# Optimization experiments

Measured on AMD Instinct MI355X. Metric: run time of the kernel, lower is better.

## Reference

```python
import jax, jax.numpy as jnp
import numpy as np

N, K, DN, DA, H = 20000, 16, 128, 128, 256
D_IN = DN + DA  # 256


def _lin_init(key, out_dim, in_dim):
    scale = 1.0 / np.sqrt(in_dim)
    return jax.random.uniform(key, (out_dim, in_dim), jnp.float32, -scale, scale)


def setup_inputs() -> dict:
    key = jax.random.key(0)
    ks = jax.random.split(key, 16)
    # adjacency: col 0 = parent index; cols 1..K = neighbor indices, -1 padded.
    parent = jax.random.randint(ks[0], (N, 1), 0, N, dtype=jnp.int32)
    nbr_first = jax.random.randint(ks[1], (N, 1), 0, N, dtype=jnp.int32)  # guarantee >=1 nbr
    nbr_rest = jax.random.randint(ks[2], (N, K - 1), -1, N, dtype=jnp.int32)
    adj = jnp.concatenate([parent, nbr_first, nbr_rest], axis=1)
    names = jax.random.normal(ks[3], (N, DN), jnp.float32)
    attrs = jax.random.normal(ks[4], (N, DA), jnp.float32)
    return {
        "nodeAdjacencySpecTensor": adj,
        "nodeNamesEncoded": names,
        "nodeAttributesEncoded": attrs,
        "W_in": _lin_init(ks[5], H, D_IN),
        "b_in": jnp.zeros((H,), jnp.float32),
        "W_parent": _lin_init(ks[6], H, H),
        "b_parent": jnp.zeros((H,), jnp.float32),
        "W_neighbor": _lin_init(ks[7], H, H),
        "b_neighbor": jnp.zeros((H,), jnp.float32),
        "W_ih": _lin_init(ks[8], 3 * H, H),
        "b_ih": jnp.zeros((3 * H,), jnp.float32),
        "W_hh": _lin_init(ks[9], 3 * H, H),
        "b_hh": jnp.zeros((3 * H,), jnp.float32),
        "depth": 3,
    }


def _gru_cell(x, h, W_ih, b_ih, W_hh, b_hh):
    # torch.nn.GRUCell math; gate order r, z, n.
    gi = x @ W_ih.T + b_ih
    gh = h @ W_hh.T + b_hh
    i_r, i_z, i_n = jnp.split(gi, 3, axis=-1)
    h_r, h_z, h_n = jnp.split(gh, 3, axis=-1)
    r = jax.nn.sigmoid(i_r + h_r)
    z = jax.nn.sigmoid(i_z + h_z)
    n = jnp.tanh(i_n + r * h_n)
    return (1.0 - z) * n + z * h


def reference(nodeAdjacencySpecTensor, nodeNamesEncoded, nodeAttributesEncoded,
              W_in, b_in, W_parent, b_parent, W_neighbor, b_neighbor,
              W_ih, b_ih, W_hh, b_hh, depth):
    adj = nodeAdjacencySpecTensor
    parent_idx = adj[:, 0]                 # [N]
    nbr_idx = adj[:, 1:]                   # [N, K], -1 padded
    mask = (nbr_idx >= 0)                  # [N, K]
    safe_nbr = jnp.clip(nbr_idx, 0, None)
    nbr_count = jnp.maximum(mask.sum(axis=1), 1).astype(jnp.float32)  # [N]

    node_info = jnp.concatenate([nodeNamesEncoded, nodeAttributesEncoded], axis=-1)
    x = node_info @ W_in.T + b_in          # [N, H]

    for _ in range(depth):
        p = x @ W_parent.T + b_parent      # [N, H]
        nbr = x @ W_neighbor.T + b_neighbor  # [N, H]
        # irregular gathers
        parent_feat = p[parent_idx]        # [N, H]
        gathered = nbr[safe_nbr]           # [N, K, H]
        nbr_sum = jnp.sum(gathered * mask[:, :, None], axis=1)  # [N, H]
        summary = parent_feat + nbr_sum / nbr_count[:, None]
        x = _gru_cell(x, summary, W_ih, b_ih, W_hh, b_hh)
    return x
```

## Files before the change

kernel.cpp:

```cpp
#include <hip/hip_runtime.h>
#include <hip/hip_bf16.h>

typedef __bf16 bf16x8 __attribute__((ext_vector_type(8)));
typedef __bf16 bf16x4 __attribute__((ext_vector_type(4)));
typedef float  f32x4  __attribute__((ext_vector_type(4)));

#define NN   20000
#define NADJ 17

__device__ __forceinline__ void xcd_remap(int b, int nwg, int col_shift, int& r, int& c)
{
    int q = nwg >> 3, rem = nwg & 7;
    int x = b & 7, k = b >> 3;
    int start = x * q + (x < rem ? x : rem);
    int idx = start + k;
    r = idx >> col_shift;
    c = idx & ((1 << col_shift) - 1);
}

__global__ void pack_weights_kernel(const float* __restrict__ Win, const float* __restrict__ bin,
                                    const float* __restrict__ Wp,  const float* __restrict__ bp,
                                    const float* __restrict__ Wn,  const float* __restrict__ bn,
                                    const float* __restrict__ Wih, const float* __restrict__ bih,
                                    const float* __restrict__ Whh, const float* __restrict__ bhh,
                                    __bf16* __restrict__ Wb, float* __restrict__ bc)
{
    int idx = blockIdx.x * 256 + threadIdx.x;
    if (idx < 1536) {
        int c = idx; float v;
        if (c < 256)      v = bin[c];
        else if (c < 512) { int j = c - 256; v = bp[j] + bn[j]; }
        else {
            int rel = c - 512;
            int j = (rel >> 6) * 16 + (rel & 15);
            int g = (rel >> 4) & 3;
            if      (g == 0) v = bih[j] + bhh[j];
            else if (g == 1) v = bih[256 + j] + bhh[256 + j];
            else if (g == 2) v = bih[512 + j];
            else             v = bhh[512 + j];
        }
        bc[c] = v;
    }
    if (idx >= 180224) return;
    int e = idx << 2;
    const float* src = nullptr;
    bool zero = false;
    if (e < 65536) {
        int row = e >> 8, k = e & 255;
        src = Win + (size_t)row * 256 + k;
    } else if (e < 196608) {
        int rel = e - 65536;
        int row = rel >> 9, k = rel & 511;
        src = (k < 256) ? (Wp + (size_t)row * 256 + k)
                        : (Wn + (size_t)row * 256 + (k - 256));
    } else {
        int rel = e - 196608;
        int row = rel >> 9, k = rel & 511;
        int j = (row >> 6) * 16 + (row & 15);
        int g = (row >> 4) & 3;
        if (k < 256) {
            if (g == 3) zero = true;
            else {
                int off = (g == 0) ? 0 : (g == 1) ? 256 : 512;
                src = Wih + (size_t)(off + j) * 256 + k;
            }
        } else {
            int k2 = k - 256;
            if (g == 2) zero = true;
            else {
                int off = (g == 0) ? 0 : (g == 1) ? 256 : 512;
                src = Whh + (size_t)(off + j) * 256 + k2;
            }
        }
    }
    float4 v = zero ? make_float4(0.f, 0.f, 0.f, 0.f) : *(const float4*)src;
    bf16x4 o = { (__bf16)v.x, (__bf16)v.y, (__bf16)v.z, (__bf16)v.w };
    *(bf16x4*)(Wb + (size_t)e) = o;
}

__global__ void pack_info_kernel(const float* __restrict__ names, const float* __restrict__ attrs,
                                 __bf16* __restrict__ xb)
{
    int idx = blockIdx.x * 256 + threadIdx.x;
    if (idx >= NN * 64) return;
    int i  = idx >> 6;
    int d4 = (idx & 63) << 2;
    const float* src = (d4 < 128) ? (names + (size_t)i * 128 + d4)
                                  : (attrs + (size_t)i * 128 + (d4 - 128));
    float4 v = *(const float4*)src;
    bf16x4 o = { (__bf16)v.x, (__bf16)v.y, (__bf16)v.z, (__bf16)v.w };
    *(bf16x4*)(xb + (size_t)i * 256 + d4) = o;
}

__global__ void gather_avg_kernel(const int* __restrict__ adj, const __bf16* __restrict__ x,
                                  __bf16* __restrict__ G2)
{
    const int l  = threadIdx.x & 63;
    const int w  = threadIdx.x >> 6;
    const int lh = l & 31;
    const int node = blockIdx.x * 8 + w * 2 + (l >> 5);
    int av = (lh < NADJ) ? adj[(size_t)node * NADJ + lh] : -1;
    float s[8] = {0.f, 0.f, 0.f, 0.f, 0.f, 0.f, 0.f, 0.f};
    int cnt = 0;
#pragma unroll
    for (int j = 1; j < NADJ; ++j) {
        int idx = __shfl(av, (l & 32) + j, 64);
        if (idx >= 0) {
            ++cnt;
            bf16x8 v = *(const bf16x8*)(x + (size_t)idx * 256 + lh * 8);
#pragma unroll
            for (int u = 0; u < 8; ++u) s[u] += (float)v[u];
        }
    }
    float inv = 1.f / (float)(cnt < 1 ? 1 : cnt);
    bf16x8 o;
#pragma unroll
    for (int u = 0; u < 8; ++u) o[u] = (__bf16)(s[u] * inv);
    *(bf16x8*)(G2 + (size_t)node * 256 + lh * 8) = o;
}

#define PIPE_BARRIER()                                \
    do {                                              \
        asm volatile("" ::: "memory");                \
        __builtin_amdgcn_s_barrier();                 \
        asm volatile("" ::: "memory");                \
    } while (0)

__global__ __launch_bounds__(512, 4)
void gemm_bias_kernel(const __bf16* __restrict__ A0, const __bf16* __restrict__ A1, int lda,
                      const int* __restrict__ parents, int par_stride,
                      const __bf16* __restrict__ W, int ldw,
                      const float* __restrict__ bias,
                      __bf16* __restrict__ Cb, __bf16* __restrict__ Cl,
                      int n_rows, int n_cols, int kt_n, int nwg, int col_shift)
{
    __shared__ __align__(16) __bf16 As[2][128 * 64];
    __shared__ __align__(16) __bf16 Bs[2][128 * 64];
    __shared__ int par_s[128];
    const int t = threadIdx.x;
    const int w = t >> 6;
    const int l = t & 63;
    int rb, cb_;
    xcd_remap(blockIdx.x, nwg, col_shift, rb, cb_);
    const int brow = rb * 128;
    const int bcol = cb_ * 128;
    const int wr = (w >> 1) * 32, wc = (w & 1) * 64;

    if (parents) {
        if (t < 128) {
            int node = brow + t; if (node > n_rows - 1) node = n_rows - 1;
            par_s[t] = parents[(size_t)node * par_stride];
        }
        __syncthreads();
    }

    auto stage = [&](int kt, int buf) {
        const int k0 = kt * 64;
#pragma unroll
        for (int i = 0; i < 2; ++i) {
            int f   = i * 512 + t;
            int row = f >> 3;
            int cs  = ((f & 7) * 16) ^ ((row & 7) << 4);
            int ar  = brow + row; if (ar > n_rows - 1) ar = n_rows - 1;
            const __bf16* abase;
            if (parents && k0 < 256)             abase = A0 + (size_t)par_s[row] * 256 + k0;
            else if (A1 != nullptr && k0 >= 256) abase = A1 + (size_t)ar * 256 + (k0 - 256);
            else                                 abase = A0 + (size_t)ar * lda + k0;
            const __bf16* ga = abase + (cs >> 1);
            char* la = (char*)As[buf] + (i * 512 + w * 64) * 16;
            __builtin_amdgcn_global_load_lds(
                (const __attribute__((address_space(1))) unsigned int*)ga,
                (__attribute__((address_space(3))) unsigned int*)la, 16, 0, 0);
        }
#pragma unroll
        for (int i = 0; i < 2; ++i) {
            int f   = i * 512 + t;
            int row = f >> 3;
            int cs  = ((f & 7) * 16) ^ ((row & 7) << 4);
            const __bf16* gb = W + (size_t)(bcol + row) * ldw + k0 + (cs >> 1);
            char* lb = (char*)Bs[buf] + (i * 512 + w * 64) * 16;
            __builtin_amdgcn_global_load_lds(
                (const __attribute__((address_space(1))) unsigned int*)gb,
                (__attribute__((address_space(3))) unsigned int*)lb, 16, 0, 0);
        }
    };

    f32x4 acc[2][4] = {};
    stage(0, 0);

    for (int kt = 0; kt < kt_n; ++kt) {
        const int buf = kt & 1;
        if (kt + 1 < kt_n) {
            stage(kt + 1, buf ^ 1);
            asm volatile("s_waitcnt vmcnt(4)" ::: "memory");
        } else {
            asm volatile("s_waitcnt vmcnt(0)" ::: "memory");
        }
        PIPE_BARRIER();
#pragma unroll
        for (int ks = 0; ks < 2; ++ks) {
            bf16x8 af[2], bfv[4];
#pragma unroll
            for (int m = 0; m < 2; ++m) {
                int row = wr + m * 16 + (l & 15);
                int cb  = (ks * 64 + ((l >> 4) * 16)) ^ ((row & 7) << 4);
                af[m] = *(const bf16x8*)((const char*)As[buf] + row * 128 + cb);
            }
#pragma unroll
            for (int n = 0; n < 4; ++n) {
                int row = wc + n * 16 + (l & 15);
                int cb  = (ks * 64 + ((l >> 4) * 16)) ^ ((row & 7) << 4);
                bfv[n] = *(const bf16x8*)((const char*)Bs[buf] + row * 128 + cb);
            }
#pragma unroll
            for (int m = 0; m < 2; ++m)
#pragma unroll
                for (int n = 0; n < 4; ++n)
                    acc[m][n] = __builtin_amdgcn_mfma_f32_16x16x32_bf16(af[m], bfv[n], acc[m][n], 0, 0, 0);
        }
        PIPE_BARRIER();
    }
#pragma unroll
    for (int m = 0; m < 2; ++m) {
        int r0 = brow + wr + m * 16 + ((l >> 4) * 4);
#pragma unroll
        for (int n = 0; n < 4; ++n) {
            int c = bcol + wc + n * 16 + (l & 15);
            float bv = bias[c];
#pragma unroll
            for (int i = 0; i < 4; ++i) {
                int r = r0 + i;
                if (r < n_rows) {
                    float v = acc[m][n][i] + bv;
                    __bf16 hi = (__bf16)v;
                    Cb[(size_t)r * n_cols + c] = hi;
                    if (Cl) Cl[(size_t)r * n_cols + c] = (__bf16)(v - (float)hi);
                }
            }
        }
    }
}

__global__ __launch_bounds__(512, 4)
void gru_gemm_kernel(const __bf16* __restrict__ A0, const __bf16* __restrict__ A1,
                     const __bf16* __restrict__ W,
                     const float* __restrict__ bias,
                     const __bf16* __restrict__ sbh, const __bf16* __restrict__ sbl,
                     float* __restrict__ X, __bf16* __restrict__ xb_next,
                     int n_rows)
{
    __shared__ __align__(16) __bf16 As[2][128 * 64];
    __shared__ __align__(16) __bf16 Bs[2][128 * 64];
    const int t = threadIdx.x;
    const int w = t >> 6;
    const int l = t & 63;
    int rb, cb_;
    xcd_remap(blockIdx.x, 157 * 8, 3, rb, cb_);
    const int brow = rb * 128;
    const int bcol = cb_ * 128;
    const int wr = (w >> 1) * 32, wc = (w & 1) * 64;

    auto stage = [&](int kt, int buf) {
        const int k0 = kt * 64;
        const __bf16* ab = (kt < 4) ? (A0 + k0) : (A1 + (k0 - 256));
#pragma unroll
        for (int i = 0; i < 2; ++i) {
            int f   = i * 512 + t;
            int row = f >> 3;
            int cs  = ((f & 7) * 16) ^ ((row & 7) << 4);
            int ar  = brow + row; if (ar > n_rows - 1) ar = n_rows - 1;
            const __bf16* ga = ab + (size_t)ar * 256 + (cs >> 1);
            char* la = (char*)As[buf] + (i * 512 + w * 64) * 16;
            __builtin_amdgcn_global_load_lds(
                (const __attribute__((address_space(1))) unsigned int*)ga,
                (__attribute__((address_space(3))) unsigned int*)la, 16, 0, 0);
        }
#pragma unroll
        for (int i = 0; i < 2; ++i) {
            int f   = i * 512 + t;
            int row = f >> 3;
            int cs  = ((f & 7) * 16) ^ ((row & 7) << 4);
            const __bf16* gb = W + (size_t)(bcol + row) * 512 + k0 + (cs >> 1);
            char* lb = (char*)Bs[buf] + (i * 512 + w * 64) * 16;
            __builtin_amdgcn_global_load_lds(
                (const __attribute__((address_space(1))) unsigned int*)gb,
                (__attribute__((address_space(3))) unsigned int*)lb, 16, 0, 0);
        }
    };

    f32x4 acc[2][4] = {};
    stage(0, 0);

    for (int kt = 0; kt < 8; ++kt) {
        const int buf = kt & 1;
        const int skipn = (kt < 4) ? 3 : 2;
        if (kt < 7) {
            stage(kt + 1, buf ^ 1);
            asm volatile("s_waitcnt vmcnt(4)" ::: "memory");
        } else {
            asm volatile("s_waitcnt vmcnt(0)" ::: "memory");
        }
        PIPE_BARRIER();
#pragma unroll
        for (int ks = 0; ks < 2; ++ks) {
            bf16x8 af[2], bfv[4];
#pragma unroll
            for (int m = 0; m < 2; ++m) {
                int row = wr + m * 16 + (l & 15);
                int cb  = (ks * 64 + ((l >> 4) * 16)) ^ ((row & 7) << 4);
                af[m] = *(const bf16x8*)((const char*)As[buf] + row * 128 + cb);
            }
#pragma unroll
            for (int n = 0; n < 4; ++n) {
                if (n == skipn) continue;
                int row = wc + n * 16 + (l & 15);
                int cb  = (ks * 64 + ((l >> 4) * 16)) ^ ((row & 7) << 4);
                bfv[n] = *(const bf16x8*)((const char*)Bs[buf] + row * 128 + cb);
            }
#pragma unroll
            for (int m = 0; m < 2; ++m)
#pragma unroll
                for (int n = 0; n < 4; ++n)
                    if (n != skipn)
                        acc[m][n] = __builtin_amdgcn_mfma_f32_16x16x32_bf16(af[m], bfv[n], acc[m][n], 0, 0, 0);
        }
        PIPE_BARRIER();
    }

    const int jb = ((bcol + wc) >> 6) * 16 + (l & 15);
    const int c0 = bcol + wc + (l & 15);
    const float b0 = bias[c0], b1 = bias[c0 + 16], b2 = bias[c0 + 32], b3 = bias[c0 + 48];
#pragma unroll
    for (int m = 0; m < 2; ++m) {
        int r0 = brow + wr + m * 16 + ((l >> 4) * 4);
#pragma unroll
        for (int i = 0; i < 4; ++i) {
            int r = r0 + i;
            if (r < n_rows) {
                float gr  = acc[m][0][i] + b0;
                float gz  = acc[m][1][i] + b1;
                float gin = acc[m][2][i] + b2;
                float ghn = acc[m][3][i] + b3;
                float rg = 1.f / (1.f + __expf(-gr));
                float zg = 1.f / (1.f + __expf(-gz));
                float a2 = gin + rg * ghn;
                float tt = __expf(-2.f * fabsf(a2));
                float ng = (1.f - tt) / (1.f + tt);
                ng = (a2 < 0.f) ? -ng : ng;
                float h = (float)sbh[(size_t)r * 256 + jb] + (float)sbl[(size_t)r * 256 + jb];
                float out = (1.f - zg) * ng + zg * h;
                if (X)       X[(size_t)r * 256 + jb] = out;
                if (xb_next) xb_next[(size_t)r * 256 + jb] = (__bf16)out;
            }
        }
    }
}

extern "C" void kernel_launch(void* const* d_in, const int* in_sizes, int n_in,
                              void* d_out, int out_size, void* d_ws, size_t ws_size,
                              hipStream_t stream)
{
    const int*   adj   = (const int*)  d_in[0];
    const float* names = (const float*)d_in[1];
    const float* attrs = (const float*)d_in[2];
    const float* Win = (const float*)d_in[3];
    const float* bin = (const float*)d_in[4];
    const float* Wp  = (const float*)d_in[5];
    const float* bp  = (const float*)d_in[6];
    const float* Wn  = (const float*)d_in[7];
    const float* bn  = (const float*)d_in[8];
    const float* Wih = (const float*)d_in[9];
    const float* bih = (const float*)d_in[10];
    const float* Whh = (const float*)d_in[11];
    const float* bhh = (const float*)d_in[12];
    float* X = (float*)d_out;

    char* w = (char*)d_ws;
    __bf16* xinfo = (__bf16*)(w);
    __bf16* xb0   = (__bf16*)(w + 10240000);
    __bf16* xb1   = (__bf16*)(w + 20480000);
    __bf16* sbh   = (__bf16*)(w + 30720000);
    __bf16* sbl   = (__bf16*)(w + 40960000);
    __bf16* G2    = (__bf16*)(w + 51200000);
    __bf16* Wb    = (__bf16*)(w + 61440000);
    float*  bc    = (float*) (w + 62881792);

    pack_weights_kernel<<<704, 256, 0, stream>>>(Win, bin, Wp, bp, Wn, bn, Wih, bih, Whh, bhh, Wb, bc);
    pack_info_kernel<<<5000, 256, 0, stream>>>(names, attrs, xinfo);

    gemm_bias_kernel<<<314, 512, 0, stream>>>(xinfo, nullptr, 256, nullptr, 0,
                                              Wb, 256, bc, xb0, nullptr, NN, 256, 4, 314, 1);

    __bf16* cur = xb0;
    __bf16* nxt = xb1;
    for (int d = 0; d < 3; ++d) {
        gather_avg_kernel<<<2500, 256, 0, stream>>>(adj, cur, G2);
        gemm_bias_kernel<<<314, 512, 0, stream>>>(cur, G2, 256, adj, NADJ,
                                                  Wb + 65536, 512, bc + 256,
                                                  sbh, sbl, NN, 256, 8, 314, 1);
        gru_gemm_kernel<<<1256, 512, 0, stream>>>(cur, sbh, Wb + 196608, bc + 512,
                                                  sbh, sbl, (d == 2) ? X : nullptr,
                                                  (d < 2) ? nxt : nullptr, NN);
        __bf16* tmp = cur; cur = nxt; nxt = tmp;
    }
}
```

Before: 224.1 us.

## Make GRU GEMM persistent with cross-tile prefetch and merge packing kernels

The GRU gate GEMM now launches 512 blocks, and each block loops over up to three 128x128 output tiles in a single pipelined stream of k-steps. The next tile's first stage is prefetched while the current tile's last step is computed, and the epilogue runs inline before the accumulators are reset. This aims to cut per-block prologue and pipeline-drain cost and the wave tail. The two input-packing kernels are also fused into one launch to remove a kernel launch. Load imbalance remains, since some blocks process three tiles and others two, and the in-loop epilogue may raise register pressure.

Measured after the change: 241.4 us. 1.08x slower.

```diff
diff --git a/kernel.cpp b/kernel.cpp
--- a/kernel.cpp
+++ b/kernel.cpp
@@ -18,13 +18,27 @@
     c = idx & ((1 << col_shift) - 1);
 }
 
-__global__ void pack_weights_kernel(const float* __restrict__ Win, const float* __restrict__ bin,
-                                    const float* __restrict__ Wp,  const float* __restrict__ bp,
-                                    const float* __restrict__ Wn,  const float* __restrict__ bn,
-                                    const float* __restrict__ Wih, const float* __restrict__ bih,
-                                    const float* __restrict__ Whh, const float* __restrict__ bhh,
-                                    __bf16* __restrict__ Wb, float* __restrict__ bc)
-{
+__global__ void pack_all_kernel(const float* __restrict__ Win, const float* __restrict__ bin,
+                                const float* __restrict__ Wp,  const float* __restrict__ bp,
+                                const float* __restrict__ Wn,  const float* __restrict__ bn,
+                                const float* __restrict__ Wih, const float* __restrict__ bih,
+                                const float* __restrict__ Whh, const float* __restrict__ bhh,
+                                const float* __restrict__ names, const float* __restrict__ attrs,
+                                __bf16* __restrict__ Wb, float* __restrict__ bc,
+                                __bf16* __restrict__ xb)
+{
+    if (blockIdx.x >= 704) {
+        int idx = (blockIdx.x - 704) * 256 + threadIdx.x;
+        if (idx >= NN * 64) return;
+        int i  = idx >> 6;
+        int d4 = (idx & 63) << 2;
+        const float* src = (d4 < 128) ? (names + (size_t)i * 128 + d4)
+                                      : (attrs + (size_t)i * 128 + (d4 - 128));
+        float4 v = *(const float4*)src;
+        bf16x4 o = { (__bf16)v.x, (__bf16)v.y, (__bf16)v.z, (__bf16)v.w };
+        *(bf16x4*)(xb + (size_t)i * 256 + d4) = o;
+        return;
+    }
     int idx = blockIdx.x * 256 + threadIdx.x;
     if (idx < 1536) {
         int c = idx; float v;
@@ -41,7 +55,6 @@
         }
         bc[c] = v;
     }
-    if (idx >= 180224) return;
     int e = idx << 2;
     const float* src = nullptr;
     bool zero = false;
@@ -78,20 +91,6 @@
     *(bf16x4*)(Wb + (size_t)e) = o;
 }
 
-__global__ void pack_info_kernel(const float* __restrict__ names, const float* __restrict__ attrs,
-                                 __bf16* __restrict__ xb)
-{
-    int idx = blockIdx.x * 256 + threadIdx.x;
-    if (idx >= NN * 64) return;
-    int i  = idx >> 6;
-    int d4 = (idx & 63) << 2;
-    const float* src = (d4 < 128) ? (names + (size_t)i * 128 + d4)
-                                  : (attrs + (size_t)i * 128 + (d4 - 128));
-    float4 v = *(const float4*)src;
-    bf16x4 o = { (__bf16)v.x, (__bf16)v.y, (__bf16)v.z, (__bf16)v.w };
-    *(bf16x4*)(xb + (size_t)i * 256 + d4) = o;
-}
-
 __global__ void gather_avg_kernel(const int* __restrict__ adj, const __bf16* __restrict__ x,
                                   __bf16* __restrict__ G2)
 {
@@ -254,14 +253,21 @@
     const int t = threadIdx.x;
     const int w = t >> 6;
     const int l = t & 63;
-    int rb, cb_;
-    xcd_remap(blockIdx.x, 157 * 8, 3, rb, cb_);
-    const int brow = rb * 128;
-    const int bcol = cb_ * 128;
     const int wr = (w >> 1) * 32, wc = (w & 1) * 64;
 
-    auto stage = [&](int kt, int buf) {
+    int browA[3], bcolA[3];
+    int nt = 0;
+    for (int tt = blockIdx.x; tt < 157 * 8; tt += 512) {
+        int rb, cb_;
+        xcd_remap(tt, 157 * 8, 3, rb, cb_);
+        browA[nt] = rb * 128;
+        bcolA[nt] = cb_ * 128;
+        ++nt;
+    }
+
+    auto stage = [&](int ti, int kt, int buf) {
         const int k0 = kt * 64;
+        const int brow = browA[ti], bcol = bcolA[ti];
         const __bf16* ab = (kt < 4) ? (A0 + k0) : (A1 + (k0 - 256));
 #pragma unroll
         for (int i = 0; i < 2; ++i) {
@@ -289,13 +295,16 @@
     };
 
     f32x4 acc[2][4] = {};
-    stage(0, 0);
-
-    for (int kt = 0; kt < 8; ++kt) {
-        const int buf = kt & 1;
+    const int total = nt * 8;
+    stage(0, 0, 0);
+
+    for (int g = 0; g < total; ++g) {
+        const int buf = g & 1;
+        const int kt  = g & 7;
+        const int ti  = g >> 3;
         const int skipn = (kt < 4) ? 3 : 2;
-        if (kt < 7) {
-            stage(kt + 1, buf ^ 1);
+        if (g + 1 < total) {
+            stage((g + 1) >> 3, (g + 1) & 7, buf ^ 1);
             asm volatile("s_waitcnt vmcnt(4)" ::: "memory");
         } else {
             asm volatile("s_waitcnt vmcnt(0)" ::: "memory");
@@ -325,33 +334,41 @@
                         acc[m][n] = __builtin_amdgcn_mfma_f32_16x16x32_bf16(af[m], bfv[n], acc[m][n], 0, 0, 0);
         }
         PIPE_BARRIER();
-    }
-
-    const int jb = ((bcol + wc) >> 6) * 16 + (l & 15);
-    const int c0 = bcol + wc + (l & 15);
-    const float b0 = bias[c0], b1 = bias[c0 + 16], b2 = bias[c0 + 32], b3 = bias[c0 + 48];
-#pragma unroll
-    for (int m = 0; m < 2; ++m) {
-        int r0 = brow + wr + m * 16 + ((l >> 4) * 4);
-#pragma unroll
-        for (int i = 0; i < 4; ++i) {
-            int r = r0 + i;
-            if (r < n_rows) {
-                float gr  = acc[m][0][i] + b0;
-                float gz  = acc[m][1][i] + b1;
-                float gin = acc[m][2][i] + b2;
-                float ghn = acc[m][3][i] + b3;
-                float rg = 1.f / (1.f + __expf(-gr));
-                float zg = 1.f / (1.f + __expf(-gz));
-                float a2 = gin + rg * ghn;
-                float tt = __expf(-2.f * fabsf(a2));
-                float ng = (1.f - tt) / (1.f + tt);
-                ng = (a2 < 0.f) ? -ng : ng;
-                float h = (float)sbh[(size_t)r * 256 + jb] + (float)sbl[(size_t)r * 256 + jb];
-                float out = (1.f - zg) * ng + zg * h;
-                if (X)       X[(size_t)r * 256 + jb] = out;
-                if (xb_next) xb_next[(size_t)r * 256 + jb] = (__bf16)out;
-            }
+
+        if (kt == 7) {
+            const int brow = browA[ti], bcol = bcolA[ti];
+            const int jb = ((bcol + wc) >> 6) * 16 + (l & 15);
+            const int c0 = bcol + wc + (l & 15);
+            const float b0 = bias[c0], b1 = bias[c0 + 16], b2 = bias[c0 + 32], b3 = bias[c0 + 48];
+#pragma unroll
+            for (int m = 0; m < 2; ++m) {
+                int r0 = brow + wr + m * 16 + ((l >> 4) * 4);
+#pragma unroll
+                for (int i = 0; i < 4; ++i) {
+                    int r = r0 + i;
+                    if (r < n_rows) {
+                        float gr  = acc[m][0][i] + b0;
+                        float gz  = acc[m][1][i] + b1;
+                        float gin = acc[m][2][i] + b2;
+                        float ghn = acc[m][3][i] + b3;
+                        float rg = 1.f / (1.f + __expf(-gr));
+                        float zg = 1.f / (1.f + __expf(-gz));
+                        float a2 = gin + rg * ghn;
+                        float tt = __expf(-2.f * fabsf(a2));
+                        float ng = (1.f - tt) / (1.f + tt);
+                        ng = (a2 < 0.f) ? -ng : ng;
+                        float h = (float)sbh[(size_t)r * 256 + jb] + (float)sbl[(size_t)r * 256 + jb];
+                        float out = (1.f - zg) * ng + zg * h;
+                        if (X)       X[(size_t)r * 256 + jb] = out;
+                        if (xb_next) xb_next[(size_t)r * 256 + jb] = (__bf16)out;
+                    }
+                }
+            }
+#pragma unroll
+            for (int m = 0; m < 2; ++m)
+#pragma unroll
+                for (int n = 0; n < 4; ++n)
+                    acc[m][n] = (f32x4){0.f, 0.f, 0.f, 0.f};
         }
     }
 }
@@ -385,8 +402,8 @@
     __bf16* Wb    = (__bf16*)(w + 61440000);
     float*  bc    = (float*) (w + 62881792);
 
-    pack_weights_kernel<<<704, 256, 0, stream>>>(Win, bin, Wp, bp, Wn, bn, Wih, bih, Whh, bhh, Wb, bc);
-    pack_info_kernel<<<5000, 256, 0, stream>>>(names, attrs, xinfo);
+    pack_all_kernel<<<5704, 256, 0, stream>>>(Win, bin, Wp, bp, Wn, bn, Wih, bih, Whh, bhh,
+                                              names, attrs, Wb, bc, xinfo);
 
     gemm_bias_kernel<<<314, 512, 0, stream>>>(xinfo, nullptr, 256, nullptr, 0,
                                               Wb, 256, bc, xb0, nullptr, NN, 256, 4, 314, 1);
@@ -398,9 +415,9 @@
         gemm_bias_kernel<<<314, 512, 0, stream>>>(cur, G2, 256, adj, NADJ,
                                                   Wb + 65536, 512, bc + 256,
                                                   sbh, sbl, NN, 256, 8, 314, 1);
-        gru_gemm_kernel<<<1256, 512, 0, stream>>>(cur, sbh, Wb + 196608, bc + 512,
-                                                  sbh, sbl, (d == 2) ? X : nullptr,
-                                                  (d < 2) ? nxt : nullptr, NN);
+        gru_gemm_kernel<<<512, 512, 0, stream>>>(cur, sbh, Wb + 196608, bc + 512,
+                                                 sbh, sbl, (d == 2) ? X : nullptr,
+                                                 (d < 2) ? nxt : nullptr, NN);
         __bf16* tmp = cur; cur = nxt; nxt = tmp;
     }
 }
```
